# Optimization experiments

Hardware: AMD Instinct MI355X
Metric: run time of the kernel (lower is better)

Reference implementation:

```python
import jax, jax.numpy as jnp
import numpy as np

B, T, F, H, C = 256, 14, 1024, 1024, 2513


def lstm_step(Wih, Whh, bih, bhh, x, h, c):
    # PyTorch LSTM cell: gate order i, f, g, o
    g = x @ Wih.T + bih + h @ Whh.T + bhh
    i, f, gg, o = jnp.split(g, 4, axis=-1)
    i = jax.nn.sigmoid(i)
    f = jax.nn.sigmoid(f)
    gg = jnp.tanh(gg)
    o = jax.nn.sigmoid(o)
    c = f * c + i * gg
    h = o * jnp.tanh(c)
    return h, c


def setup_inputs() -> dict:
    key = jax.random.key(0)
    ks = jax.random.split(key, 11)
    s = 1.0 / np.sqrt(H)
    u = lambda k, shape: jax.random.uniform(k, shape, jnp.float32, -s, s)
    return {
        "inputs": jax.random.normal(ks[0], (B, T, F), jnp.float32),
        "roll_Wih": u(ks[1], (4 * H, F)),
        "roll_Whh": u(ks[2], (4 * H, H)),
        "roll_bih": u(ks[3], (4 * H,)),
        "roll_bhh": u(ks[4], (4 * H,)),
        "unroll_Wih": u(ks[5], (4 * H, F)),
        "unroll_Whh": u(ks[6], (4 * H, H)),
        "unroll_bih": u(ks[7], (4 * H,)),
        "unroll_bhh": u(ks[8], (4 * H,)),
        "cls_W": u(ks[9], (C, H)),
        "cls_b": u(ks[10], (C,)),
    }


def reference(inputs, roll_Wih, roll_Whh, roll_bih, roll_bhh,
              unroll_Wih, unroll_Whh, unroll_bih, unroll_bhh, cls_W, cls_b):
    x_t = jnp.transpose(inputs, (1, 0, 2))  # [T, B, F]

    # Rolling LSTM: scan over time, keep hidden/cell at every step
    h0 = jnp.zeros((B, H), inputs.dtype)
    c0 = jnp.zeros((B, H), inputs.dtype)

    def roll(carry, xt):
        h, c = carry
        h, c = lstm_step(roll_Wih, roll_Whh, roll_bih, roll_bhh, xt, h, c)
        return (h, c), (h, c)

    _, (hs, cs) = jax.lax.scan(roll, (h0, c0), x_t)  # each [T, B, H]

    # Unrolling LSTM: for each t, feed inputs[t] repeated (T - t + 1) times,
    # starting from (hs[t], cs[t]). Vectorized over t: run T+1 steps for all
    # branches with constant per-branch input x_t[t], then pick step (T - t).
    def unroll(carry, _):
        h, c = carry  # [T, B, H]
        h, c = lstm_step(unroll_Wih, unroll_Whh, unroll_bih, unroll_bhh, x_t, h, c)
        return (h, c), h

    _, h_all = jax.lax.scan(unroll, (hs, cs), None, length=T + 1)  # [T+1, T, B, H]
    t_idx = jnp.arange(T)
    h_n = h_all[T - t_idx, t_idx]  # [T, B, H], last output of each branch

    x = jnp.transpose(h_n, (1, 0, 2))  # [B, T, H]
    y = x @ cls_W.T + cls_b  # [B, T, C]
    return y
```

## Files before the change

### kernel.cpp

```cpp
#include <hip/hip_runtime.h>

#define DEVFN __device__ __forceinline__

typedef __bf16 bf16x8 __attribute__((ext_vector_type(8)));
typedef float floatx4 __attribute__((ext_vector_type(4)));
typedef unsigned short us4 __attribute__((ext_vector_type(4)));


DEVFN unsigned short f2bf(float x) {
    union { float f; unsigned u; } v; v.f = x;
    v.u += 0x7FFFu + ((v.u >> 16) & 1u);
    return (unsigned short)(v.u >> 16);
}

DEVFN float bf2f(unsigned short s) {
    union { unsigned u; float f; } v; v.u = ((unsigned)s) << 16; return v.f;
}

DEVFN float sigm(float x) { return 1.f / (1.f + __expf(-x)); }
DEVFN float tanh_fast(float x) { float t = __expf(2.f * x); return 1.f - 2.f / (t + 1.f); }

DEVFN void gload_lds16(const unsigned short* g, unsigned short* l) {
    __builtin_amdgcn_global_load_lds(
        (__attribute__((address_space(1))) unsigned int*)g,
        (__attribute__((address_space(3))) unsigned int*)l, 16, 0, 0);
}

#define CFENCE asm volatile("" ::: "memory")


__global__ __launch_bounds__(256) void transpose_bt(const float* __restrict__ in,
                                                    unsigned short* __restrict__ out) {
    int idx = blockIdx.x * 256 + threadIdx.x;
    int k4 = (idx & 255) << 2;
    int row = idx >> 8;
    int t = row >> 8, b = row & 255;
    float4 v = *(const float4*)(in + (size_t)(b * 14 + t) * 1024 + k4);
    us4 o = {f2bf(v.x), f2bf(v.y), f2bf(v.z), f2bf(v.w)};
    *(us4*)(out + (size_t)row * 1024 + k4) = o;
}

__global__ __launch_bounds__(256) void conv_w4(const float* __restrict__ s0, const float* __restrict__ s1,
                                               const float* __restrict__ s2, const float* __restrict__ s3,
                                               unsigned short* __restrict__ d0, unsigned short* __restrict__ d1,
                                               unsigned short* __restrict__ d2, unsigned short* __restrict__ d3) {
    int t = blockIdx.x * 256 + threadIdx.x;
    int which = t >> 20;
    int off = (t & 1048575) << 2;
    const float* s = (which == 0) ? s0 : (which == 1) ? s1 : (which == 2) ? s2 : s3;
    unsigned short* d = (which == 0) ? d0 : (which == 1) ? d1 : (which == 2) ? d2 : d3;
    float4 v = *(const float4*)(s + off);
    us4 o = {f2bf(v.x), f2bf(v.y), f2bf(v.z), f2bf(v.w)};
    *(us4*)(d + off) = o;
}

__global__ __launch_bounds__(256) void conv_cls(const float* __restrict__ in,
                                                unsigned short* __restrict__ out) {
    int t = blockIdx.x * 256 + threadIdx.x;
    int off = t << 2;
    us4 o = {0, 0, 0, 0};
    if (off < 2573312) {
        float4 v = *(const float4*)(in + off);
        o = (us4){f2bf(v.x), f2bf(v.y), f2bf(v.z), f2bf(v.w)};
    }
    *(us4*)(out + off) = o;
}

__global__ __launch_bounds__(256) void bias_interleave(const float* __restrict__ a,
                                                       const float* __restrict__ b,
                                                       float* __restrict__ o4, int n) {
    int i = blockIdx.x * 256 + threadIdx.x;
    if (i < n) {
        int g = i >> 10, h = i & 1023;
        o4[h * 4 + g] = a[i] + b[i];
    }
}

__global__ __launch_bounds__(256) void cell_only(const unsigned short* __restrict__ pre4b,
                                                 float* __restrict__ c_out,
                                                 unsigned short* __restrict__ h_out) {
    int idx = blockIdx.x * 256 + threadIdx.x;
    us4 pv = *(const us4*)(pre4b + (size_t)idx * 4);
    float iv = sigm(bf2f(pv.x)), fv = sigm(bf2f(pv.y));
    float gv = tanh_fast(bf2f(pv.z)), ov = sigm(bf2f(pv.w));
    float cn = iv * gv;
    float hn = ov * tanh_fast(cn);
    c_out[idx] = cn;
    h_out[idx] = f2bf(hn);
}

template <int MODE>
__global__ __launch_bounds__(256)
void lstm_big(const unsigned short* __restrict__ A1, const unsigned short* __restrict__ W1,
              const unsigned short* __restrict__ pre4b,
              const float* __restrict__ bias4,
              const float* __restrict__ c_in,
              float* __restrict__ c_out,
              unsigned short* __restrict__ h_out,
              unsigned short* __restrict__ h_alt, int retire_t,
              unsigned short* __restrict__ gout_bf,
              const float* __restrict__ clsb,
              float* __restrict__ outp, int gx) {
    __shared__ __align__(16) unsigned short lds[2][8192];

    const int tid = threadIdx.x;
    const int nwg = gridDim.x;
    int id = blockIdx.x;
    id = ((id & 7) * (nwg >> 3)) + (id >> 3);
    const int bx = id % gx;
    const int by = id / gx;
    const int m0 = by * 128;
    const int n0h = bx * 32;
    const int n0c = bx * 128;
    const int lane = tid & 63;
    const int wv = tid >> 6;
    const int wm = wv >> 1, wn = wv & 1;
    const int r16 = lane & 15;
    const int kg = lane >> 4;

    auto stage = [&](int u, int buf) {
        const int ko = u * 32;
#pragma unroll
        for (int is = 0; is < 2; ++is) {
            int c = is * 256 + tid;
            int row = c >> 2, kq = c & 3;
            int kqg = kq ^ ((row >> 1) & 3);
            gload_lds16(A1 + (size_t)(m0 + row) * 1024 + ko + kqg * 8, &lds[buf][c * 8]);
        }
#pragma unroll
        for (int is = 0; is < 2; ++is) {
            int c = is * 256 + tid;
            int row = c >> 2, kq = c & 3;
            int kqg = kq ^ ((row >> 1) & 3);
            int wr;
            if (MODE == 2) wr = n0c + row;
            else wr = ((row >> 4) & 3) * 1024 + n0h + ((row >> 6) << 4) + (row & 15);
            gload_lds16(W1 + (size_t)wr * 1024 + ko + kqg * 8, &lds[buf][4096 + c * 8]);
        }
    };

    floatx4 acc[4][4];
#pragma unroll
    for (int i = 0; i < 4; ++i)
#pragma unroll
        for (int j = 0; j < 4; ++j) acc[i][j] = {0.f, 0.f, 0.f, 0.f};

    stage(0, 0);
    stage(1, 1);
    asm volatile("s_waitcnt vmcnt(4)" ::: "memory");
    __builtin_amdgcn_s_barrier();
    CFENCE;

#pragma unroll 2
    for (int u = 0; u < 32; ++u) {
        const int cur = u & 1;
        bf16x8 a[4], b[4];
#pragma unroll
        for (int i = 0; i < 4; ++i) {
            int row = wm * 64 + i * 16 + r16;
            a[i] = *(const bf16x8*)&lds[cur][row * 32 + (kg ^ ((row >> 1) & 3)) * 8];
        }
#pragma unroll
        for (int j = 0; j < 4; ++j) {
            int row = wn * 64 + j * 16 + r16;
            b[j] = *(const bf16x8*)&lds[cur][4096 + row * 32 + (kg ^ ((row >> 1) & 3)) * 8];
        }
        __builtin_amdgcn_s_setprio(1);
#pragma unroll
        for (int i = 0; i < 4; ++i)
#pragma unroll
            for (int j = 0; j < 4; ++j)
                acc[i][j] = __builtin_amdgcn_mfma_f32_16x16x32_bf16(a[i], b[j], acc[i][j], 0, 0, 0);
        __builtin_amdgcn_s_setprio(0);

        if (u < 31) {
            __builtin_amdgcn_s_barrier();
            if (u < 30) {
                stage(u + 2, cur);
                asm volatile("s_waitcnt vmcnt(4)" ::: "memory");
            } else {
                asm volatile("s_waitcnt vmcnt(0)" ::: "memory");
            }
            __builtin_amdgcn_s_barrier();
            CFENCE;
        }
    }

    if (MODE == 2) {
#pragma unroll
        for (int i = 0; i < 4; ++i)
#pragma unroll
            for (int j = 0; j < 4; ++j)
#pragma unroll
                for (int rg = 0; rg < 4; ++rg) {
                    int m = m0 + wm * 64 + i * 16 + kg * 4 + rg;
                    int gn = n0c + wn * 64 + j * 16 + r16;
                    if (gn < 2513) {
                        int bb = m & 255, tt = m >> 8;
                        outp[(size_t)(bb * 14 + tt) * 2513 + gn] = acc[i][j][rg] + clsb[gn];
                    }
                }
        return;
    }

    const int h = n0h + wn * 16 + r16;
    float4 bv = make_float4(0.f, 0.f, 0.f, 0.f);
    if (MODE == 3 && bias4) bv = *(const float4*)(bias4 + (size_t)h * 4);
    unsigned short* hw = h_out;
    if (MODE == 1 && (m0 >> 8) == retire_t) hw = h_alt;

#pragma unroll
    for (int i = 0; i < 4; ++i)
#pragma unroll
        for (int rg = 0; rg < 4; ++rg) {
            int m = m0 + wm * 64 + i * 16 + kg * 4 + rg;
            size_t mh = (size_t)m * 1024 + h;
            float gi_ = acc[i][0][rg] + bv.x;
            float gf_ = acc[i][1][rg] + bv.y;
            float gg_ = acc[i][2][rg] + bv.z;
            float go_ = acc[i][3][rg] + bv.w;
            if (MODE == 3) {
                us4 o = {f2bf(gi_), f2bf(gf_), f2bf(gg_), f2bf(go_)};
                *(us4*)(gout_bf + mh * 4) = o;
            } else {
                us4 pv = *(const us4*)(pre4b + mh * 4);
                gi_ += bf2f(pv.x); gf_ += bf2f(pv.y);
                gg_ += bf2f(pv.z); go_ += bf2f(pv.w);
                float co = c_in[mh];
                float iv = sigm(gi_), fv = sigm(gf_);
                float gv = tanh_fast(gg_), ov = sigm(go_);
                float cn = fv * co + iv * gv;
                float hn = ov * tanh_fast(cn);
                c_out[mh] = cn;
                hw[mh] = f2bf(hn);
            }
        }
}

__global__ __launch_bounds__(256)
void lstm_small(const unsigned short* __restrict__ A1, const unsigned short* __restrict__ W1,
                const unsigned short* __restrict__ pre4b,
                const float* __restrict__ c_in,
                float* __restrict__ c_out,
                unsigned short* __restrict__ h_out,
                unsigned short* __restrict__ h_alt, int retire_t,
                int gx) {
    constexpr int ATILE = 32 * 64;
    constexpr int LOADS = 5;

    __shared__ __align__(16) unsigned short lds[4][ATILE + 8192];

    const int tid = threadIdx.x;
    const int nwg = gridDim.x;
    int id = blockIdx.x;
    id = ((id & 7) * (nwg >> 3)) + (id >> 3);
    const int bx = id % gx;
    const int by = id / gx;
    const int m0 = by * 32;
    const int n0 = bx * 32;
    const int lane = tid & 63;
    const int wv = tid >> 6;
    const int wm = wv >> 1, wn = wv & 1;
    const int r16 = lane & 15;
    const int kg = lane >> 4;

    auto stage = [&](int kt, int buf) {
        const int ko = kt * 64;
        {
            int c = tid;
            int row = c >> 3, kq = c & 7, kqg = kq ^ (row & 7);
            gload_lds16(A1 + (size_t)(m0 + row) * 1024 + ko + kqg * 8, &lds[buf][c * 8]);
        }
#pragma unroll
        for (int is = 0; is < 4; ++is) {
            int c = is * 256 + tid;
            int row = c >> 3, kq = c & 7, kqg = kq ^ (row & 7);
            int wr = ((row >> 4) & 3) * 1024 + n0 + ((row >> 6) << 4) + (row & 15);
            gload_lds16(W1 + (size_t)wr * 1024 + ko + kqg * 8, &lds[buf][ATILE + c * 8]);
        }
    };

    floatx4 acc[4];
#pragma unroll
    for (int j = 0; j < 4; ++j) acc[j] = {0.f, 0.f, 0.f, 0.f};

    stage(0, 0);
    stage(1, 1);
    stage(2, 2);
    asm volatile("s_waitcnt vmcnt(%0)" :: "n"(2 * LOADS) : "memory");
    __builtin_amdgcn_s_barrier();
    CFENCE;

#pragma unroll 4
    for (int u = 0; u < 16; ++u) {
        const int cur = u & 3;
#pragma unroll
        for (int kk = 0; kk < 2; ++kk) {
            bf16x8 a, b[4];
            const int kqg = kk * 4 + kg;
            {
                int row = wm * 16 + r16;
                a = *(const bf16x8*)&lds[cur][row * 64 + (kqg ^ (row & 7)) * 8];
            }
#pragma unroll
            for (int j = 0; j < 4; ++j) {
                int row = wn * 64 + j * 16 + r16;
                b[j] = *(const bf16x8*)&lds[cur][ATILE + row * 64 + (kqg ^ (row & 7)) * 8];
            }
#pragma unroll
            for (int j = 0; j < 4; ++j)
                acc[j] = __builtin_amdgcn_mfma_f32_16x16x32_bf16(a, b[j], acc[j], 0, 0, 0);
        }
        if (u < 15) {
            __builtin_amdgcn_s_barrier();
            if (u < 13) {
                stage(u + 3, (u + 3) & 3);
                asm volatile("s_waitcnt vmcnt(%0)" :: "n"(2 * LOADS) : "memory");
            } else if (u == 13) {
                asm volatile("s_waitcnt vmcnt(%0)" :: "n"(LOADS) : "memory");
            } else {
                asm volatile("s_waitcnt vmcnt(0)" ::: "memory");
            }
            __builtin_amdgcn_s_barrier();
            CFENCE;
        }
    }

    const int h = n0 + wn * 16 + r16;
    unsigned short* hw = h_out;
    if ((m0 >> 8) == retire_t) hw = h_alt;

#pragma unroll
    for (int rg = 0; rg < 4; ++rg) {
        int m = m0 + wm * 16 + kg * 4 + rg;
        size_t mh = (size_t)m * 1024 + h;
        us4 pv = *(const us4*)(pre4b + mh * 4);
        float gi_ = acc[0][rg] + bf2f(pv.x);
        float gf_ = acc[1][rg] + bf2f(pv.y);
        float gg_ = acc[2][rg] + bf2f(pv.z);
        float go_ = acc[3][rg] + bf2f(pv.w);
        float co = c_in[mh];
        float iv = sigm(gi_), fv = sigm(gf_);
        float gv = tanh_fast(gg_), ov = sigm(go_);
        float cn = fv * co + iv * gv;
        float hn = ov * tanh_fast(cn);
        c_out[mh] = cn;
        hw[mh] = f2bf(hn);
    }
}


extern "C" void kernel_launch(void* const* d_in, const int* in_sizes, int n_in,
                              void* d_out, int out_size, void* d_ws, size_t ws_size,
                              hipStream_t stream) {
    (void)in_sizes; (void)n_in; (void)out_size; (void)ws_size;
    const float* inputs   = (const float*)d_in[0];
    const float* roll_Wih = (const float*)d_in[1];
    const float* roll_Whh = (const float*)d_in[2];
    const float* roll_bih = (const float*)d_in[3];
    const float* roll_bhh = (const float*)d_in[4];
    const float* un_Wih   = (const float*)d_in[5];
    const float* un_Whh   = (const float*)d_in[6];
    const float* un_bih   = (const float*)d_in[7];
    const float* un_bhh   = (const float*)d_in[8];
    const float* cls_Wf   = (const float*)d_in[9];
    const float* cls_b    = (const float*)d_in[10];
    float* out = (float*)d_out;

    char* ws = (char*)d_ws;
    size_t off = 0;
    auto alloc = [&](size_t bytes) -> char* {
        char* p = ws + off;
        off += (bytes + 255) & ~(size_t)255;
        return p;
    };
    unsigned short* xt   = (unsigned short*)alloc(3584ull * 1024 * 2);
    unsigned short* rWih = (unsigned short*)alloc(4096ull * 1024 * 2);
    unsigned short* rWhh = (unsigned short*)alloc(4096ull * 1024 * 2);
    unsigned short* uWih = (unsigned short*)alloc(4096ull * 1024 * 2);
    unsigned short* uWhh = (unsigned short*)alloc(4096ull * 1024 * 2);
    unsigned short* cWp  = (unsigned short*)alloc(2560ull * 1024 * 2);
    float* rbias4 = (float*)alloc(1024 * 4 * 4);
    float* ubias4 = (float*)alloc(1024 * 4 * 4);
    unsigned short* XpreB  = (unsigned short*)alloc(3584ull * 4096 * 2);
    unsigned short* XrollB = (unsigned short*)alloc(3584ull * 4096 * 2);
    float* uc     = (float*)alloc(3584ull * 1024 * 4);
    unsigned short* hb0    = (unsigned short*)alloc(3584ull * 1024 * 2);
    unsigned short* hb1    = (unsigned short*)alloc(3584ull * 1024 * 2);
    unsigned short* hfinal = (unsigned short*)alloc(3584ull * 1024 * 2);

    const size_t SF = 256 * 1024;

    transpose_bt<<<3584, 256, 0, stream>>>(inputs, xt);
    conv_w4<<<16384, 256, 0, stream>>>(roll_Wih, roll_Whh, un_Wih, un_Whh,
                                       rWih, rWhh, uWih, uWhh);
    conv_cls<<<2560, 256, 0, stream>>>(cls_Wf, cWp);
    bias_interleave<<<16, 256, 0, stream>>>(roll_bih, roll_bhh, rbias4, 4096);
    bias_interleave<<<16, 256, 0, stream>>>(un_bih, un_bhh, ubias4, 4096);

    lstm_big<3><<<896, 256, 0, stream>>>(
        xt, uWih, nullptr, ubias4, nullptr, nullptr, nullptr, nullptr, -1,
        XpreB, nullptr, nullptr, 32);
    lstm_big<3><<<896, 256, 0, stream>>>(
        xt, rWih, nullptr, rbias4, nullptr, nullptr, nullptr, nullptr, -1,
        XrollB, nullptr, nullptr, 32);

    cell_only<<<1024, 256, 0, stream>>>(XrollB, uc, hb0);
    for (int t = 1; t < 14; ++t) {
        lstm_small<<<256, 256, 0, stream>>>(
            hb0 + (size_t)(t - 1) * SF, rWhh,
            XrollB + (size_t)t * SF * 4,
            uc + (size_t)(t - 1) * SF, uc + (size_t)t * SF,
            hb0 + (size_t)t * SF, nullptr, -1, 32);
    }

    for (int s = 0; s <= 14; ++s) {
        int nb = (15 - s < 14) ? (15 - s) : 14;
        int M = nb * 256;
        const unsigned short* hsrc = (s & 1) ? hb1 : hb0;
        unsigned short* hdst = (s & 1) ? hb0 : hb1;
        int rt = (s >= 1) ? (14 - s) : -1;
        if (M >= 1024) {
            lstm_big<1><<<32 * (M / 128), 256, 0, stream>>>(
                hsrc, uWhh, XpreB, nullptr, uc, uc, hdst, hfinal, rt,
                nullptr, nullptr, nullptr, 32);
        } else {
            lstm_small<<<32 * (M / 32), 256, 0, stream>>>(
                hsrc, uWhh, XpreB, uc, uc, hdst, hfinal, rt, 32);
        }
    }

    lstm_big<2><<<560, 256, 0, stream>>>(
        hfinal, cWp, nullptr, nullptr, nullptr, nullptr, nullptr, nullptr, -1,
        nullptr, cls_b, out, 20);
}
```

Measured before the change: 821.9 us.

## Template GEMM N-tile width and use 128x256 tiles for large LSTM GEMMs

Makes the lstm_big kernel templated on the hidden-column width per block (NH), so a block can compute 64 hidden units (256 gate rows) instead of 32. The input-projection GEMMs, the large unroll steps (M>=2304) and the classifier use the wider tile with half as many blocks, raising arithmetic intensity and A-tile reuse per block. It also adds launch_bounds min-blocks=2. The cost is double the accumulator registers and more LDS per block, which could lower occupancy or cause spills, and fewer blocks for the smaller grids.

```diff
diff --git a/kernel.cpp b/kernel.cpp
--- a/kernel.cpp
+++ b/kernel.cpp
@@ -89,8 +89,8 @@
     h_out[idx] = f2bf(hn);
 }
 
-template <int MODE>
-__global__ __launch_bounds__(256)
+template <int MODE, int NH>
+__global__ __launch_bounds__(256, 2)
 void lstm_big(const unsigned short* __restrict__ A1, const unsigned short* __restrict__ W1,
               const unsigned short* __restrict__ pre4b,
               const float* __restrict__ bias4,
@@ -101,7 +101,15 @@
               unsigned short* __restrict__ gout_bf,
               const float* __restrict__ clsb,
               float* __restrict__ outp, int gx) {
-    __shared__ __align__(16) unsigned short lds[2][8192];
+    constexpr int BROWS = 4 * NH;
+    constexpr int FN = BROWS / 32;
+    constexpr int BISS = BROWS / 64;
+    constexpr int LOADS = 2 + BISS;
+    constexpr int ASH = 4096;
+    constexpr int BSH = BROWS * 32;
+    constexpr int HH = NH / 32;
+
+    __shared__ __align__(16) unsigned short lds[2][ASH + BSH];
 
     const int tid = threadIdx.x;
     const int nwg = gridDim.x;
@@ -110,8 +118,8 @@
     const int bx = id % gx;
     const int by = id / gx;
     const int m0 = by * 128;
-    const int n0h = bx * 32;
-    const int n0c = bx * 128;
+    const int n0h = bx * NH;
+    const int n0c = bx * BROWS;
     const int lane = tid & 63;
     const int wv = tid >> 6;
     const int wm = wv >> 1, wn = wv & 1;
@@ -128,48 +136,48 @@
             gload_lds16(A1 + (size_t)(m0 + row) * 1024 + ko + kqg * 8, &lds[buf][c * 8]);
         }
 #pragma unroll
-        for (int is = 0; is < 2; ++is) {
+        for (int is = 0; is < BISS; ++is) {
             int c = is * 256 + tid;
             int row = c >> 2, kq = c & 3;
             int kqg = kq ^ ((row >> 1) & 3);
             int wr;
             if (MODE == 2) wr = n0c + row;
             else wr = ((row >> 4) & 3) * 1024 + n0h + ((row >> 6) << 4) + (row & 15);
-            gload_lds16(W1 + (size_t)wr * 1024 + ko + kqg * 8, &lds[buf][4096 + c * 8]);
+            gload_lds16(W1 + (size_t)wr * 1024 + ko + kqg * 8, &lds[buf][ASH + c * 8]);
         }
     };
 
-    floatx4 acc[4][4];
+    floatx4 acc[4][FN];
 #pragma unroll
     for (int i = 0; i < 4; ++i)
 #pragma unroll
-        for (int j = 0; j < 4; ++j) acc[i][j] = {0.f, 0.f, 0.f, 0.f};
+        for (int j = 0; j < FN; ++j) acc[i][j] = {0.f, 0.f, 0.f, 0.f};
 
     stage(0, 0);
     stage(1, 1);
-    asm volatile("s_waitcnt vmcnt(4)" ::: "memory");
+    asm volatile("s_waitcnt vmcnt(%0)" :: "n"(LOADS) : "memory");
     __builtin_amdgcn_s_barrier();
     CFENCE;
 
 #pragma unroll 2
     for (int u = 0; u < 32; ++u) {
         const int cur = u & 1;
-        bf16x8 a[4], b[4];
+        bf16x8 a[4], b[FN];
 #pragma unroll
         for (int i = 0; i < 4; ++i) {
             int row = wm * 64 + i * 16 + r16;
             a[i] = *(const bf16x8*)&lds[cur][row * 32 + (kg ^ ((row >> 1) & 3)) * 8];
         }
 #pragma unroll
-        for (int j = 0; j < 4; ++j) {
-            int row = wn * 64 + j * 16 + r16;
-            b[j] = *(const bf16x8*)&lds[cur][4096 + row * 32 + (kg ^ ((row >> 1) & 3)) * 8];
+        for (int j = 0; j < FN; ++j) {
+            int row = wn * (BROWS / 2) + j * 16 + r16;
+            b[j] = *(const bf16x8*)&lds[cur][ASH + row * 32 + (kg ^ ((row >> 1) & 3)) * 8];
         }
         __builtin_amdgcn_s_setprio(1);
 #pragma unroll
         for (int i = 0; i < 4; ++i)
 #pragma unroll
-            for (int j = 0; j < 4; ++j)
+            for (int j = 0; j < FN; ++j)
                 acc[i][j] = __builtin_amdgcn_mfma_f32_16x16x32_bf16(a[i], b[j], acc[i][j], 0, 0, 0);
         __builtin_amdgcn_s_setprio(0);
 
@@ -177,7 +185,7 @@
             __builtin_amdgcn_s_barrier();
             if (u < 30) {
                 stage(u + 2, cur);
-                asm volatile("s_waitcnt vmcnt(4)" ::: "memory");
+                asm volatile("s_waitcnt vmcnt(%0)" :: "n"(LOADS) : "memory");
             } else {
                 asm volatile("s_waitcnt vmcnt(0)" ::: "memory");
             }
@@ -190,11 +198,11 @@
 #pragma unroll
         for (int i = 0; i < 4; ++i)
 #pragma unroll
-            for (int j = 0; j < 4; ++j)
+            for (int j = 0; j < FN; ++j)
 #pragma unroll
                 for (int rg = 0; rg < 4; ++rg) {
                     int m = m0 + wm * 64 + i * 16 + kg * 4 + rg;
-                    int gn = n0c + wn * 64 + j * 16 + r16;
+                    int gn = n0c + wn * (BROWS / 2) + j * 16 + r16;
                     if (gn < 2513) {
                         int bb = m & 255, tt = m >> 8;
                         outp[(size_t)(bb * 14 + tt) * 2513 + gn] = acc[i][j][rg] + clsb[gn];
@@ -203,38 +211,41 @@
         return;
     }
 
-    const int h = n0h + wn * 16 + r16;
-    float4 bv = make_float4(0.f, 0.f, 0.f, 0.f);
-    if (MODE == 3 && bias4) bv = *(const float4*)(bias4 + (size_t)h * 4);
     unsigned short* hw = h_out;
     if (MODE == 1 && (m0 >> 8) == retire_t) hw = h_alt;
 
 #pragma unroll
-    for (int i = 0; i < 4; ++i)
-#pragma unroll
-        for (int rg = 0; rg < 4; ++rg) {
-            int m = m0 + wm * 64 + i * 16 + kg * 4 + rg;
-            size_t mh = (size_t)m * 1024 + h;
-            float gi_ = acc[i][0][rg] + bv.x;
-            float gf_ = acc[i][1][rg] + bv.y;
-            float gg_ = acc[i][2][rg] + bv.z;
-            float go_ = acc[i][3][rg] + bv.w;
-            if (MODE == 3) {
-                us4 o = {f2bf(gi_), f2bf(gf_), f2bf(gg_), f2bf(go_)};
-                *(us4*)(gout_bf + mh * 4) = o;
-            } else {
-                us4 pv = *(const us4*)(pre4b + mh * 4);
-                gi_ += bf2f(pv.x); gf_ += bf2f(pv.y);
-                gg_ += bf2f(pv.z); go_ += bf2f(pv.w);
-                float co = c_in[mh];
-                float iv = sigm(gi_), fv = sigm(gf_);
-                float gv = tanh_fast(gg_), ov = sigm(go_);
-                float cn = fv * co + iv * gv;
-                float hn = ov * tanh_fast(cn);
-                c_out[mh] = cn;
-                hw[mh] = f2bf(hn);
+    for (int hh = 0; hh < HH; ++hh) {
+        const int h = n0h + wn * (NH / 2) + hh * 16 + r16;
+        float4 bv = make_float4(0.f, 0.f, 0.f, 0.f);
+        if (MODE == 3 && bias4) bv = *(const float4*)(bias4 + (size_t)h * 4);
+#pragma unroll
+        for (int i = 0; i < 4; ++i)
+#pragma unroll
+            for (int rg = 0; rg < 4; ++rg) {
+                int m = m0 + wm * 64 + i * 16 + kg * 4 + rg;
+                size_t mh = (size_t)m * 1024 + h;
+                float gi_ = acc[i][hh * 4 + 0][rg] + bv.x;
+                float gf_ = acc[i][hh * 4 + 1][rg] + bv.y;
+                float gg_ = acc[i][hh * 4 + 2][rg] + bv.z;
+                float go_ = acc[i][hh * 4 + 3][rg] + bv.w;
+                if (MODE == 3) {
+                    us4 o = {f2bf(gi_), f2bf(gf_), f2bf(gg_), f2bf(go_)};
+                    *(us4*)(gout_bf + mh * 4) = o;
+                } else {
+                    us4 pv = *(const us4*)(pre4b + mh * 4);
+                    gi_ += bf2f(pv.x); gf_ += bf2f(pv.y);
+                    gg_ += bf2f(pv.z); go_ += bf2f(pv.w);
+                    float co = c_in[mh];
+                    float iv = sigm(gi_), fv = sigm(gf_);
+                    float gv = tanh_fast(gg_), ov = sigm(go_);
+                    float cn = fv * co + iv * gv;
+                    float hn = ov * tanh_fast(cn);
+                    c_out[mh] = cn;
+                    hw[mh] = f2bf(hn);
+                }
             }
-        }
+    }
 }
 
 __global__ __launch_bounds__(256)
@@ -398,12 +409,12 @@
     bias_interleave<<<16, 256, 0, stream>>>(roll_bih, roll_bhh, rbias4, 4096);
     bias_interleave<<<16, 256, 0, stream>>>(un_bih, un_bhh, ubias4, 4096);
 
-    lstm_big<3><<<896, 256, 0, stream>>>(
+    lstm_big<3, 64><<<448, 256, 0, stream>>>(
         xt, uWih, nullptr, ubias4, nullptr, nullptr, nullptr, nullptr, -1,
-        XpreB, nullptr, nullptr, 32);
-    lstm_big<3><<<896, 256, 0, stream>>>(
+        XpreB, nullptr, nullptr, 16);
+    lstm_big<3, 64><<<448, 256, 0, stream>>>(
         xt, rWih, nullptr, rbias4, nullptr, nullptr, nullptr, nullptr, -1,
-        XrollB, nullptr, nullptr, 32);
+        XrollB, nullptr, nullptr, 16);
 
     cell_only<<<1024, 256, 0, stream>>>(XrollB, uc, hb0);
     for (int t = 1; t < 14; ++t) {
@@ -420,17 +431,21 @@
         const unsigned short* hsrc = (s & 1) ? hb1 : hb0;
         unsigned short* hdst = (s & 1) ? hb0 : hb1;
         int rt = (s >= 1) ? (14 - s) : -1;
-        if (M >= 1024) {
-            lstm_big<1><<<32 * (M / 128), 256, 0, stream>>>(
+        if (M >= 2304) {
+            lstm_big<1, 64><<<M / 8, 256, 0, stream>>>(
+                hsrc, uWhh, XpreB, nullptr, uc, uc, hdst, hfinal, rt,
+                nullptr, nullptr, nullptr, 16);
+        } else if (M >= 1024) {
+            lstm_big<1, 32><<<M / 4, 256, 0, stream>>>(
                 hsrc, uWhh, XpreB, nullptr, uc, uc, hdst, hfinal, rt,
                 nullptr, nullptr, nullptr, 32);
         } else {
-            lstm_small<<<32 * (M / 32), 256, 0, stream>>>(
+            lstm_small<<<M, 256, 0, stream>>>(
                 hsrc, uWhh, XpreB, uc, uc, hdst, hfinal, rt, 32);
         }
     }
 
-    lstm_big<2><<<560, 256, 0, stream>>>(
+    lstm_big<2, 64><<<280, 256, 0, stream>>>(
         hfinal, cWp, nullptr, nullptr, nullptr, nullptr, nullptr, nullptr, -1,
-        nullptr, cls_b, out, 20);
-}
+        nullptr, cls_b, out, 10);
+}
```

After: 782.9 us. 1.05x faster.
